# Kernel tuning notes

Hardware: AMD Instinct MI355X
Metric: run time of the kernel (lower is better)

Reference implementation:

```python
import jax, jax.numpy as jnp
from jax import lax
import numpy as np

DIM = 384; NH = 8; N = 16; K = 4; DIN = 768; DTR = 24  # d_model, heads, d_state, d_conv, d_inner, dt_rank
B = 8; Hh = 48; Ww = 48


def _ln(x, g, b):
    m = jnp.mean(x, -1, keepdims=True)
    v = jnp.mean((x - m) ** 2, -1, keepdims=True)
    return (x - m) / jnp.sqrt(v + 1e-5) * g + b


def _mamba(x, in_w, in_b, conv_w, conv_b, xp_w, dt_w, dt_b, A_log, Dp, out_w, out_b):
    # x: (B, L, DIM)
    Bb, L, _ = x.shape
    xz = x @ in_w.T + in_b                      # (B, L, 2*DIN)
    xm, z = xz[..., :DIN], xz[..., DIN:]
    # depthwise causal conv over sequence
    xc = jnp.pad(xm.transpose(0, 2, 1), ((0, 0), (0, 0), (K - 1, 0)))  # (B, DIN, L+K-1)
    xconv = lax.conv_general_dilated(xc, conv_w[:, None, :], (1,), 'VALID',
                                     feature_group_count=DIN,
                                     dimension_numbers=('NCH', 'OIH', 'NCH'))
    u = jax.nn.silu((xconv + conv_b[None, :, None]).transpose(0, 2, 1))  # (B, L, DIN)
    dbc = u @ xp_w.T                            # (B, L, DTR + 2N)
    delta = jax.nn.softplus(dbc[..., :DTR] @ dt_w.T + dt_b)  # (B, L, DIN)
    Bm = dbc[..., DTR:DTR + N]                  # (B, L, N)
    Cm = dbc[..., DTR + N:]                     # (B, L, N)
    A = -jnp.exp(A_log)                         # (DIN, N)

    def step(h, inp):
        d_t, B_t, C_t, u_t = inp                # (B,DIN),(B,N),(B,N),(B,DIN)
        dA = jnp.exp(d_t[:, :, None] * A)       # (B, DIN, N)
        h = h * dA + d_t[:, :, None] * B_t[:, None, :] * u_t[:, :, None]
        y = jnp.einsum('bdn,bn->bd', h, C_t)
        return h, y

    h0 = jnp.zeros((Bb, DIN, N), x.dtype)
    xs = (delta.transpose(1, 0, 2), Bm.transpose(1, 0, 2), Cm.transpose(1, 0, 2), u.transpose(1, 0, 2))
    _, ys = lax.scan(step, h0, xs)
    y = ys.transpose(1, 0, 2) + u * Dp
    y = y * jax.nn.silu(z)
    return y @ out_w.T + out_b


def _forward(x, n1_g, n1_b, ap_w, ap_b, n2_g, n2_b, in_w, in_b, conv_w, conv_b, xp_w, dt_w, dt_b,
             A_log, Dp, out_w, out_b, mod_w1, mod_b1, mod_w2, mod_b2, n3_g, n3_b,
             fc1_w, fc1_b, fc2_w, fc2_b):
    Bb, C, Hc, Wc = x.shape
    xs = x.reshape(Bb, C, Hc * Wc).transpose(0, 2, 1)          # (B, L, C)
    xn = _ln(xs, n1_g, n1_b)
    attn = jax.nn.softmax(xn @ ap_w.T + ap_b, axis=1)          # softmax over sequence
    gc = jnp.einsum('bln,blc->bnc', attn, xn).mean(1)          # (B, C)
    mod = jax.nn.silu(gc @ mod_w1.T + mod_b1) @ mod_w2.T + mod_b2
    xn2 = _ln(xs, n2_g, n2_b)
    mo = _mamba(xn2, in_w, in_b, conv_w, conv_b, xp_w, dt_w, dt_b, A_log, Dp, out_w, out_b)
    mo = mo * (1.0 + mod[:, None, :])
    xs = xs + mo
    h = _ln(xs, n3_g, n3_b)
    h = jax.nn.gelu(h @ fc1_w.T + fc1_b) @ fc2_w.T + fc2_b
    xs = xs + h
    return xs.transpose(0, 2, 1).reshape(Bb, C, Hc, Wc)


def setup_inputs() -> dict:
    key = jax.random.key(0)
    ks = jax.random.split(key, 16)
    s = 0.02
    p = {}
    p['x'] = jax.random.normal(ks[0], (B, DIM, Hh, Ww), jnp.float32)
    p['n1_g'] = jnp.ones((DIM,), jnp.float32); p['n1_b'] = jnp.zeros((DIM,), jnp.float32)
    p['ap_w'] = jax.random.normal(ks[1], (NH, DIM), jnp.float32) * s; p['ap_b'] = jnp.zeros((NH,), jnp.float32)
    p['n2_g'] = jnp.ones((DIM,), jnp.float32); p['n2_b'] = jnp.zeros((DIM,), jnp.float32)
    p['in_w'] = jax.random.normal(ks[2], (2 * DIN, DIM), jnp.float32) * s; p['in_b'] = jnp.zeros((2 * DIN,), jnp.float32)
    p['conv_w'] = jax.random.normal(ks[3], (DIN, K), jnp.float32) * s; p['conv_b'] = jnp.zeros((DIN,), jnp.float32)
    p['xp_w'] = jax.random.normal(ks[4], (DTR + 2 * N, DIN), jnp.float32) * s
    p['dt_w'] = jax.random.normal(ks[5], (DIN, DTR), jnp.float32) * s
    p['dt_b'] = jax.random.uniform(ks[6], (DIN,), jnp.float32, minval=-4.0, maxval=-2.0)
    p['A_log'] = jnp.log(jnp.tile(jnp.arange(1, N + 1, dtype=jnp.float32), (DIN, 1)))
    p['Dp'] = jnp.ones((DIN,), jnp.float32)
    p['out_w'] = jax.random.normal(ks[7], (DIM, DIN), jnp.float32) * s; p['out_b'] = jnp.zeros((DIM,), jnp.float32)
    p['mod_w1'] = jax.random.normal(ks[8], (2 * DIM, DIM), jnp.float32) * s; p['mod_b1'] = jnp.zeros((2 * DIM,), jnp.float32)
    p['mod_w2'] = jax.random.normal(ks[9], (DIM, 2 * DIM), jnp.float32) * s; p['mod_b2'] = jnp.zeros((DIM,), jnp.float32)
    p['n3_g'] = jnp.ones((DIM,), jnp.float32); p['n3_b'] = jnp.zeros((DIM,), jnp.float32)
    p['fc1_w'] = jax.random.normal(ks[10], (4 * DIM, DIM), jnp.float32) * s; p['fc1_b'] = jnp.zeros((4 * DIM,), jnp.float32)
    p['fc2_w'] = jax.random.normal(ks[11], (DIM, 4 * DIM), jnp.float32) * s; p['fc2_b'] = jnp.zeros((DIM,), jnp.float32)
    return p


def reference(x, n1_g, n1_b, ap_w, ap_b, n2_g, n2_b, in_w, in_b, conv_w, conv_b, xp_w, dt_w, dt_b,
              A_log, Dp, out_w, out_b, mod_w1, mod_b1, mod_w2, mod_b2, n3_g, n3_b,
              fc1_w, fc1_b, fc2_w, fc2_b):
    return _forward(x, n1_g, n1_b, ap_w, ap_b, n2_g, n2_b, in_w, in_b, conv_w, conv_b, xp_w,
                    dt_w, dt_b, A_log, Dp, out_w, out_b, mod_w1, mod_b1, mod_w2, mod_b2,
                    n3_g, n3_b, fc1_w, fc1_b, fc2_w, fc2_b)
```

## Files before the change

kernel.cpp:

```cpp
#include <hip/hip_runtime.h>
#include <math.h>

#define DIMC 384
#define NHD 8
#define NSTATE 16
#define DINN 768
#define DTRK 24
#define BB 8
#define LSEQ 2304
#define MROWS (BB*LSEQ)
#define NCH 64
#define TCH 36
#define L2E 1.44269504f

typedef unsigned short u16;
typedef short bf16x8 __attribute__((ext_vector_type(8)));
typedef float f32x4 __attribute__((ext_vector_type(4)));

__device__ __forceinline__ float sigmoid_(float x){ return 1.f/(1.f+__expf(-x)); }
__device__ __forceinline__ float silu_(float x){ return x*sigmoid_(x); }
__device__ __forceinline__ float softplus_(float x){ return (x>20.f)?x:log1pf(__expf(x)); }
__device__ __forceinline__ float gelu_(float x){
  float x3=x*x*x;
  return 0.5f*x*(1.f+tanhf(0.7978845608028654f*(x+0.044715f*x3)));
}
__device__ __forceinline__ float bfu2f(u16 u){
  union{unsigned int i; float f;} c; c.i=((unsigned int)u)<<16; return c.f;
}
__device__ __forceinline__ u16 f2bfu(float f){
  union{float f; unsigned int i;} c; c.f=f;
  unsigned int r = c.i + 0x7FFFu + ((c.i>>16)&1u);
  return (u16)(r>>16);
}
__device__ __forceinline__ void gl_lds16(const u16* g, u16* l){
  __builtin_amdgcn_global_load_lds((__attribute__((address_space(1))) void*)g,
      (__attribute__((address_space(3))) void*)l, 16, 0, 0);
}

#define O1 589824
#define O2 688128
#define O3 983040
#define O4 1572864
#define O5 2162688
#define O6 2187264
#define OEND 2190336
__global__ void k_cvtall(const float* __restrict__ inw, const float* __restrict__ xpw,
    const float* __restrict__ outw, const float* __restrict__ fc1w,
    const float* __restrict__ fc2w, const float* __restrict__ dtw,
    u16* __restrict__ inw_b, u16* __restrict__ xpw_pad, u16* __restrict__ outw_b,
    u16* __restrict__ fc1w_b, u16* __restrict__ fc2w_b, u16* __restrict__ dtw_pad,
    float* __restrict__ gc){
  int i = blockIdx.x*256+threadIdx.x;
  if(i >= OEND) return;
  if(i < O1){ inw_b[i]=f2bfu(inw[i]); }
  else if(i < O2){ int j=i-O1; xpw_pad[j] = (j<43008)? f2bfu(xpw[j]) : (u16)0; }
  else if(i < O3){ int j=i-O2; outw_b[j]=f2bfu(outw[j]); }
  else if(i < O4){ int j=i-O3; fc1w_b[j]=f2bfu(fc1w[j]); }
  else if(i < O5){ int j=i-O4; fc2w_b[j]=f2bfu(fc2w[j]); }
  else if(i < O6){ int j=i-O5; int r=j>>5, c=j&31;
                   dtw_pad[j] = (c<DTRK)? f2bfu(dtw[r*DTRK+c]) : (u16)0; }
  else { gc[i-O6]=0.f; }
}

__global__ void k_transpose(const float* __restrict__ x, float* __restrict__ xs){
  __shared__ float tile[32][33];
  int b = blockIdx.z;
  int t0 = blockIdx.x*32, c0 = blockIdx.y*32;
  int tx = threadIdx.x, ty = threadIdx.y;
  const float* xb = x + (size_t)b*DIMC*LSEQ;
  #pragma unroll
  for(int q=0;q<4;q++)
    tile[ty+q*8][tx] = xb[(size_t)(c0+ty+q*8)*LSEQ + t0+tx];
  __syncthreads();
  float* xsb = xs + (size_t)b*LSEQ*DIMC;
  #pragma unroll
  for(int q=0;q<4;q++)
    xsb[(size_t)(t0+ty+q*8)*DIMC + c0+tx] = tile[tx][ty+q*8];
}

__global__ __launch_bounds__(64) void k_lnstats(const float* __restrict__ xs,
   const float* __restrict__ g1,const float* __restrict__ b1,
   const float* __restrict__ g2,const float* __restrict__ b2,
   const float* __restrict__ apw,const float* __restrict__ apb,
   float* __restrict__ meanr, float* __restrict__ rstdr,
   u16* __restrict__ xn2, float* __restrict__ scores){
  int row = blockIdx.x;
  int lane = threadIdx.x;
  const float* xr = xs + (size_t)row*DIMC;
  float v[6];
  float s=0.f, s2=0.f;
  #pragma unroll
  for(int i=0;i<6;i++){ v[i]=xr[lane+i*64]; s+=v[i]; s2+=v[i]*v[i]; }
  #pragma unroll
  for(int m=32;m>=1;m>>=1){ s += __shfl_xor(s,m); s2 += __shfl_xor(s2,m); }
  float mean = s*(1.f/DIMC);
  float var  = s2*(1.f/DIMC)-mean*mean;
  float rstd = rsqrtf(var+1e-5f);
  if(lane==0){ meanr[row]=mean; rstdr[row]=rstd; }
  float xv1[6];
  #pragma unroll
  for(int i=0;i<6;i++){
    int c = lane+i*64;
    float nx = (v[i]-mean)*rstd;
    xv1[i] = nx*g1[c]+b1[c];
    xn2[(size_t)row*DIMC+c] = f2bfu(nx*g2[c]+b2[c]);
  }
  #pragma unroll
  for(int h=0;h<NHD;h++){
    float p=0.f;
    #pragma unroll
    for(int i=0;i<6;i++) p += xv1[i]*apw[h*DIMC+lane+i*64];
    #pragma unroll
    for(int m=32;m>=1;m>>=1) p += __shfl_xor(p,m);
    if(lane==0) scores[(size_t)row*NHD+h]=p+apb[h];
  }
}

__global__ __launch_bounds__(256) void k_softmax_L(float* __restrict__ sc){
  int bh = blockIdx.x; int b = bh>>3, h = bh&7;
  int tid = threadIdx.x;
  __shared__ float red[8];
  const size_t base = (size_t)b*LSEQ*NHD + h;
  float mx = -1e30f;
  for(int l=tid;l<LSEQ;l+=256) mx = fmaxf(mx, sc[base + (size_t)l*NHD]);
  #pragma unroll
  for(int m=32;m>=1;m>>=1) mx = fmaxf(mx, __shfl_xor(mx,m));
  if((tid&63)==0) red[tid>>6]=mx;
  __syncthreads();
  mx = fmaxf(fmaxf(red[0],red[1]),fmaxf(red[2],red[3]));
  float sum=0.f;
  for(int l=tid;l<LSEQ;l+=256) sum += __expf(sc[base+(size_t)l*NHD]-mx);
  #pragma unroll
  for(int m=32;m>=1;m>>=1) sum += __shfl_xor(sum,m);
  if((tid&63)==0) red[4+(tid>>6)]=sum;
  __syncthreads();
  float inv = 1.f/(red[4]+red[5]+red[6]+red[7]);
  for(int l=tid;l<LSEQ;l+=256){
    size_t idx = base+(size_t)l*NHD;
    sc[idx] = __expf(sc[idx]-mx)*inv;
  }
}

__global__ void k_wpool(const float* __restrict__ attn, float* __restrict__ w){
  int i = blockIdx.x*256+threadIdx.x;
  if(i<MROWS){
    const float* a = attn+(size_t)i*NHD;
    float s=0.f;
    #pragma unroll
    for(int h=0;h<NHD;h++) s+=a[h];
    w[i]=s*0.125f;
  }
}

__global__ __launch_bounds__(384) void k_gc(const float* __restrict__ w,
    const float* __restrict__ xs, const float* __restrict__ meanr,
    const float* __restrict__ rstdr, const float* __restrict__ g1,
    const float* __restrict__ b1, float* __restrict__ gc){
  int b = blockIdx.x; int chunk = blockIdx.y; int c = threadIdx.x;
  int l0 = chunk*48;
  float acc=0.f, accw=0.f;
  for(int l=0;l<48;l++){
    int row = b*LSEQ + l0+l;
    float ww = w[row];
    acc  += ww*(xs[(size_t)row*DIMC+c]-meanr[row])*rstdr[row];
    accw += ww;
  }
  atomicAdd(&gc[b*DIMC+c], acc*g1[c]+accw*b1[c]);
}

__global__ __launch_bounds__(64) void k_mod1(const float* __restrict__ gc,
    const float* __restrict__ w1, const float* __restrict__ b1, float* __restrict__ h){
  int b = blockIdx.x; int n = blockIdx.y*64+threadIdx.x;
  const float* g = gc + b*DIMC;
  const float* wr = w1 + (size_t)n*DIMC;
  float acc=0.f;
  for(int k=0;k<DIMC;k++) acc += g[k]*wr[k];
  h[b*768+n] = silu_(acc+b1[n]);
}
__global__ __launch_bounds__(64) void k_mod2(const float* __restrict__ h,
    const float* __restrict__ w2, const float* __restrict__ b2, float* __restrict__ mod){
  int b = blockIdx.x; int n = blockIdx.y*64+threadIdx.x;
  const float* hh = h + b*768;
  const float* wr = w2 + (size_t)n*768;
  float acc=0.f;
  for(int k=0;k<768;k++) acc += hh[k]*wr[k];
  mod[b*DIMC+n] = acc+b2[n];
}

template<int EPI>
__global__ __launch_bounds__(256,4) void k_mgemm(
    const u16* __restrict__ A, const u16* __restrict__ W,
    const float* __restrict__ bias, void* __restrict__ outp,
    int K, int N, const float* __restrict__ aux, void* __restrict__ outp2)
{
  __shared__ u16 lA[2][4096];
  __shared__ u16 lB[2][4096];
  int tid = threadIdx.x;
  int m0 = blockIdx.x*128, n0 = blockIdx.y*128;
  int wid = tid>>6, lane = tid&63;
  int wr = wid>>1, wc = wid&1;
  int lrow = lane&15, lk = lane>>4;
  f32x4 acc[4][4];
  #pragma unroll
  for(int i=0;i<4;i++)
    #pragma unroll
    for(int j=0;j<4;j++){ acc[i][j][0]=0.f; acc[i][j][1]=0.f; acc[i][j][2]=0.f; acc[i][j][3]=0.f; }

  int r0 = tid & 127, k0 = tid >> 7;
  const u16* Ag0 = A + (size_t)(m0+r0)*K + k0*8;
  const u16* Ag1 = A + (size_t)(m0+r0)*K + (k0+2)*8;
  const u16* Bg0 = W + (size_t)(n0+r0)*K + k0*8;
  const u16* Bg1 = W + (size_t)(n0+r0)*K + (k0+2)*8;

  gl_lds16(Ag0, &lA[0][tid*8]);
  gl_lds16(Ag1, &lA[0][2048+tid*8]);
  gl_lds16(Bg0, &lB[0][tid*8]);
  gl_lds16(Bg1, &lB[0][2048+tid*8]);
  if(32 < K){
    gl_lds16(Ag0+32, &lA[1][tid*8]);
    gl_lds16(Ag1+32, &lA[1][2048+tid*8]);
    gl_lds16(Bg0+32, &lB[1][tid*8]);
    gl_lds16(Bg1+32, &lB[1][2048+tid*8]);
  }

  int cur = 0;
  for(int kb=0; kb<K; kb+=32){
    if(kb+32 < K) asm volatile("s_waitcnt vmcnt(4)" ::: "memory");
    else          asm volatile("s_waitcnt vmcnt(0)" ::: "memory");
    __builtin_amdgcn_s_barrier();
    bf16x8 af[4], bfr[4];
    #pragma unroll
    for(int i=0;i<4;i++){
      af[i]  = *reinterpret_cast<const bf16x8*>(&lA[cur][(lk*128 + wr*64 + i*16 + lrow)*8]);
      bfr[i] = *reinterpret_cast<const bf16x8*>(&lB[cur][(lk*128 + wc*64 + i*16 + lrow)*8]);
    }
    asm volatile("s_waitcnt lgkmcnt(0)" ::: "memory");
    __builtin_amdgcn_s_barrier();
    if(kb+64 < K){
      gl_lds16(Ag0 + kb+64, &lA[cur][tid*8]);
      gl_lds16(Ag1 + kb+64, &lA[cur][2048+tid*8]);
      gl_lds16(Bg0 + kb+64, &lB[cur][tid*8]);
      gl_lds16(Bg1 + kb+64, &lB[cur][2048+tid*8]);
    }
    #pragma unroll
    for(int i=0;i<4;i++)
      #pragma unroll
      for(int j=0;j<4;j++)
        acc[i][j] = __builtin_amdgcn_mfma_f32_16x16x32_bf16(af[i], bfr[j], acc[i][j], 0,0,0);
    cur ^= 1;
  }

  #pragma unroll
  for(int i=0;i<4;i++){
    int row = m0 + wr*64 + i*16 + lk*4;
    #pragma unroll
    for(int j=0;j<4;j++){
      int col = n0 + wc*64 + j*16 + lrow;
      float bc = bias ? bias[col] : 0.f;
      f32x4 v = acc[i][j];
      if(EPI==0){
        u16* o = (u16*)outp;
        #pragma unroll
        for(int r=0;r<4;r++) o[(size_t)(row+r)*N + col] = f2bfu(v[r]+bc);
      } else if(EPI==1){
        u16* o = (u16*)outp;
        #pragma unroll
        for(int r=0;r<4;r++) o[(size_t)(row+r)*N + col] = f2bfu(gelu_(v[r]+bc));
      } else if(EPI==2){
        float* o = (float*)outp;
        int bi = row/LSEQ;
        float sc = 1.f + aux[bi*DIMC + col];
        #pragma unroll
        for(int r=0;r<4;r++) o[(size_t)(row+r)*DIMC + col] += (v[r]+bc)*sc;
      } else if(EPI==3){
        float* o = (float*)outp;
        int bi = row/LSEQ, t = row - bi*LSEQ;
        float4 s;
        s.x = aux[(size_t)(row+0)*DIMC+col] + v[0] + bc;
        s.y = aux[(size_t)(row+1)*DIMC+col] + v[1] + bc;
        s.z = aux[(size_t)(row+2)*DIMC+col] + v[2] + bc;
        s.w = aux[(size_t)(row+3)*DIMC+col] + v[3] + bc;
        *reinterpret_cast<float4*>(&o[((size_t)(bi*DIMC+col))*LSEQ + t]) = s;
      } else if(EPI==4){
        float* o = (float*)outp;
        if(col < N){
          #pragma unroll
          for(int r=0;r<4;r++) o[(size_t)(row+r)*N + col] = v[r]+bc;
        }
      } else if(EPI==5){
        u16* o = (col < 768) ? (u16*)outp : (u16*)outp2;
        int cc = (col < 768) ? col : col - 768;
        #pragma unroll
        for(int r=0;r<4;r++) o[(size_t)(row+r)*768 + cc] = f2bfu(v[r]+bc);
      } else if(EPI==6){
        float* o = (float*)outp;
        u16* o2 = (u16*)outp2;
        #pragma unroll
        for(int r=0;r<4;r++){
          float val = v[r];
          if(col < 56) o[(size_t)(row+r)*56 + col] = val;
          if(col < 32) o2[(size_t)(row+r)*32 + col] = (col<DTRK)? f2bfu(val) : (u16)0;
        }
      } else {
        u16* o = (u16*)outp;
        #pragma unroll
        for(int r=0;r<4;r++) o[(size_t)(row+r)*N + col] = f2bfu(softplus_(v[r]+bc));
      }
    }
  }
}

__global__ void k_conv(const u16* __restrict__ xm, const float* __restrict__ cw,
                       const float* __restrict__ cb, u16* __restrict__ u){
  int idx = blockIdx.x*256+threadIdx.x;
  if(idx >= MROWS*(DINN/8)) return;
  int j = idx % (DINN/8); int r = idx / (DINN/8);
  int t = r % LSEQ; int d0 = j*8;
  float4 w4_[8];
  #pragma unroll
  for(int e=0;e<8;e++) w4_[e] = reinterpret_cast<const float4*>(cw)[d0+e];
  float acc[8];
  #pragma unroll
  for(int e=0;e<8;e++) acc[e]=cb[d0+e];
  #pragma unroll
  for(int k=0;k<4;k++){
    int tt=t+k-3;
    if(tt>=0){
      uint4 v = *reinterpret_cast<const uint4*>(&xm[(size_t)(r+k-3)*DINN + d0]);
      unsigned vv[4]={v.x,v.y,v.z,v.w};
      #pragma unroll
      for(int e=0;e<8;e++){
        u16 raw = (e&1)? (u16)(vv[e>>1]>>16) : (u16)(vv[e>>1]&0xffffu);
        float wk = (k==0)? w4_[e].x : (k==1)? w4_[e].y : (k==2)? w4_[e].z : w4_[e].w;
        acc[e] += bfu2f(raw)*wk;
      }
    }
  }
  u16 outv[8];
  #pragma unroll
  for(int e=0;e<8;e++) outv[e]=f2bfu(silu_(acc[e]));
  *reinterpret_cast<uint4*>(&u[(size_t)r*DINN+d0]) = *reinterpret_cast<const uint4*>(outv);
}

__global__ __launch_bounds__(256) void k_scan1(
  const u16* __restrict__ dt_, const u16* __restrict__ u_,
  const float* __restrict__ dbc, const float* __restrict__ alog,
  float* __restrict__ ssum, float* __restrict__ hloc)
{
  __shared__ float Bsh[TCH][16];
  int bid = blockIdx.x;
  int b = bid/(NCH*3); int rem = bid%(NCH*3); int ch = rem/3; int dblk = rem%3;
  int tid = threadIdx.x; int d = dblk*256 + tid;
  size_t rbase = (size_t)b*LSEQ + (size_t)ch*TCH;
  for(int j=tid; j<TCH*16; j+=256){
    int row=j>>4, n=j&15;
    Bsh[row][n] = dbc[(rbase+row)*56 + DTRK + n];
  }
  float Acl2[16];
  float a0 = -__expf(alog[(size_t)d*16])*L2E;
  bool fast = true;
  #pragma unroll
  for(int n=0;n<16;n++){
    Acl2[n] = -__expf(alog[(size_t)d*16+n])*L2E;
    float tgt = (float)(n+1)*a0;
    fast = fast && (fabsf(Acl2[n]-tgt) <= 1e-4f*fabsf(tgt));
  }
  float h[16];
  #pragma unroll
  for(int n=0;n<16;n++) h[n]=0.f;
  float S=0.f;
  const u16* dtp = dt_ + rbase*DINN + d;
  const u16* up  = u_  + rbase*DINN + d;
  __syncthreads();
  if(fast){
    for(int t=0;t<TCH;t++){
      float dt = bfu2f(dtp[(size_t)t*DINN]);
      float uv = bfu2f(up[(size_t)t*DINN]);
      float G = dt*uv;
      S += dt;
      float e = exp2f(dt*a0), w = e;
      const float4* b4 = (const float4*)Bsh[t];
      float4 B0=b4[0],B1=b4[1],B2=b4[2],B3=b4[3];
      float Bv[16]={B0.x,B0.y,B0.z,B0.w,B1.x,B1.y,B1.z,B1.w,
                    B2.x,B2.y,B2.z,B2.w,B3.x,B3.y,B3.z,B3.w};
      #pragma unroll
      for(int n=0;n<16;n++){ h[n] = h[n]*w + G*Bv[n]; w *= e; }
    }
  } else {
    for(int t=0;t<TCH;t++){
      float dt = bfu2f(dtp[(size_t)t*DINN]);
      float uv = bfu2f(up[(size_t)t*DINN]);
      float G = dt*uv;
      S += dt;
      const float4* b4 = (const float4*)Bsh[t];
      float4 B0=b4[0],B1=b4[1],B2=b4[2],B3=b4[3];
      float Bv[16]={B0.x,B0.y,B0.z,B0.w,B1.x,B1.y,B1.z,B1.w,
                    B2.x,B2.y,B2.z,B2.w,B3.x,B3.y,B3.z,B3.w};
      #pragma unroll
      for(int n=0;n<16;n++) h[n] = h[n]*exp2f(dt*Acl2[n]) + G*Bv[n];
    }
  }
  ssum[((size_t)b*NCH+ch)*DINN + d] = S;
  float* hp = hloc + (((size_t)b*NCH+ch)*DINN + d)*16;
  #pragma unroll
  for(int n=0;n<16;n++) hp[n] = h[n];
}

__global__ __launch_bounds__(256) void k_scan2(
  const float* __restrict__ ssum, const float* __restrict__ alog,
  float* __restrict__ hl)
{
  int gid = blockIdx.x*256+threadIdx.x;
  int n = gid & 15; int d = (gid>>4)%DINN; int b = gid/(DINN*NSTATE);
  float Acl2 = -__expf(alog[(size_t)d*16+n])*L2E;
  float hin=0.f;
  for(int ch=0; ch<NCH; ch++){
    size_t sidx = ((size_t)b*NCH+ch)*DINN + d;
    size_t idx  = sidx*16 + n;
    float a = exp2f(ssum[sidx]*Acl2);
    float hold = hl[idx];
    hl[idx] = hin;
    hin = a*hin + hold;
  }
}

__global__ __launch_bounds__(256) void k_scan3(
  const u16* __restrict__ dt_, u16* uy, const u16* __restrict__ z_,
  const float* __restrict__ dbc, const float* __restrict__ alog,
  const float* __restrict__ Dp, const float* __restrict__ hin)
{
  __shared__ float BC[TCH][32];
  int bid = blockIdx.x;
  int b = bid/(NCH*3); int rem = bid%(NCH*3); int ch = rem/3; int dblk = rem%3;
  int tid = threadIdx.x; int d = dblk*256 + tid;
  size_t rbase = (size_t)b*LSEQ + (size_t)ch*TCH;
  for(int j=tid; j<TCH*32; j+=256){
    int row=j>>5, c=j&31;
    BC[row][c] = dbc[(rbase+row)*56 + DTRK + c];
  }
  float Acl2[16], h[16];
  const float* hp = hin + (((size_t)b*NCH+ch)*DINN + d)*16;
  float a0 = -__expf(alog[(size_t)d*16])*L2E;
  bool fast = true;
  #pragma unroll
  for(int n=0;n<16;n++){
    Acl2[n] = -__expf(alog[(size_t)d*16+n])*L2E;
    float tgt = (float)(n+1)*a0;
    fast = fast && (fabsf(Acl2[n]-tgt) <= 1e-4f*fabsf(tgt));
    h[n] = hp[n];
  }
  float Dv = Dp[d];
  const u16* dtp = dt_ + rbase*DINN + d;
  u16*       uyp = uy  + rbase*DINN + d;
  const u16* zp  = z_  + rbase*DINN + d;
  __syncthreads();
  if(fast){
    for(int t=0;t<TCH;t++){
      float dt = bfu2f(dtp[(size_t)t*DINN]);
      float uv = bfu2f(uyp[(size_t)t*DINN]);
      float zv = bfu2f(zp[(size_t)t*DINN]);
      float G = dt*uv;
      float e = exp2f(dt*a0), w = e;
      const float4* bc4 = (const float4*)BC[t];
      float4 B0=bc4[0],B1=bc4[1],B2=bc4[2],B3=bc4[3];
      float4 C0=bc4[4],C1=bc4[5],C2=bc4[6],C3=bc4[7];
      float Bv[16]={B0.x,B0.y,B0.z,B0.w,B1.x,B1.y,B1.z,B1.w,
                    B2.x,B2.y,B2.z,B2.w,B3.x,B3.y,B3.z,B3.w};
      float Cv[16]={C0.x,C0.y,C0.z,C0.w,C1.x,C1.y,C1.z,C1.w,
                    C2.x,C2.y,C2.z,C2.w,C3.x,C3.y,C3.z,C3.w};
      float y0=0.f,y1=0.f,y2=0.f,y3=0.f;
      #pragma unroll
      for(int n=0;n<16;n++){
        h[n] = h[n]*w + G*Bv[n];
        w *= e;
        if((n&3)==0) y0 += h[n]*Cv[n];
        else if((n&3)==1) y1 += h[n]*Cv[n];
        else if((n&3)==2) y2 += h[n]*Cv[n];
        else y3 += h[n]*Cv[n];
      }
      float y = (y0+y1)+(y2+y3);
      uyp[(size_t)t*DINN] = f2bfu((y + uv*Dv)*silu_(zv));
    }
  } else {
    for(int t=0;t<TCH;t++){
      float dt = bfu2f(dtp[(size_t)t*DINN]);
      float uv = bfu2f(uyp[(size_t)t*DINN]);
      float zv = bfu2f(zp[(size_t)t*DINN]);
      float G = dt*uv;
      const float4* bc4 = (const float4*)BC[t];
      float4 B0=bc4[0],B1=bc4[1],B2=bc4[2],B3=bc4[3];
      float4 C0=bc4[4],C1=bc4[5],C2=bc4[6],C3=bc4[7];
      float Bv[16]={B0.x,B0.y,B0.z,B0.w,B1.x,B1.y,B1.z,B1.w,
                    B2.x,B2.y,B2.z,B2.w,B3.x,B3.y,B3.z,B3.w};
      float Cv[16]={C0.x,C0.y,C0.z,C0.w,C1.x,C1.y,C1.z,C1.w,
                    C2.x,C2.y,C2.z,C2.w,C3.x,C3.y,C3.z,C3.w};
      float y0=0.f,y1=0.f,y2=0.f,y3=0.f;
      #pragma unroll
      for(int n=0;n<16;n++){
        h[n] = h[n]*exp2f(dt*Acl2[n]) + G*Bv[n];
        if((n&3)==0) y0 += h[n]*Cv[n];
        else if((n&3)==1) y1 += h[n]*Cv[n];
        else if((n&3)==2) y2 += h[n]*Cv[n];
        else y3 += h[n]*Cv[n];
      }
      float y = (y0+y1)+(y2+y3);
      uyp[(size_t)t*DINN] = f2bfu((y + uv*Dv)*silu_(zv));
    }
  }
}

__global__ __launch_bounds__(64) void k_ln3(const float* __restrict__ xin,
    const float* __restrict__ g, const float* __restrict__ bb, u16* __restrict__ xout){
  int row = blockIdx.x;
  int lane = threadIdx.x;
  const float* xr = xin + (size_t)row*DIMC;
  float v[6];
  float s=0.f, s2=0.f;
  #pragma unroll
  for(int i=0;i<6;i++){ v[i]=xr[lane+i*64]; s+=v[i]; s2+=v[i]*v[i]; }
  #pragma unroll
  for(int m=32;m>=1;m>>=1){ s += __shfl_xor(s,m); s2 += __shfl_xor(s2,m); }
  float mean = s*(1.f/DIMC);
  float var  = s2*(1.f/DIMC)-mean*mean;
  float rstd = rsqrtf(var+1e-5f);
  #pragma unroll
  for(int i=0;i<6;i++){
    int c = lane+i*64;
    xout[(size_t)row*DIMC+c] = f2bfu((v[i]-mean)*rstd*g[c]+bb[c]);
  }
}

extern "C" void kernel_launch(void* const* d_in, const int* in_sizes, int n_in,
                              void* d_out, int out_size, void* d_ws, size_t ws_size,
                              hipStream_t stream)
{
  const float* x     = (const float*)d_in[0];
  const float* n1g   = (const float*)d_in[1];
  const float* n1b   = (const float*)d_in[2];
  const float* apw   = (const float*)d_in[3];
  const float* apb   = (const float*)d_in[4];
  const float* n2g   = (const float*)d_in[5];
  const float* n2b   = (const float*)d_in[6];
  const float* inw   = (const float*)d_in[7];
  const float* inb   = (const float*)d_in[8];
  const float* convw = (const float*)d_in[9];
  const float* convb = (const float*)d_in[10];
  const float* xpw   = (const float*)d_in[11];
  const float* dtw   = (const float*)d_in[12];
  const float* dtb   = (const float*)d_in[13];
  const float* Alog  = (const float*)d_in[14];
  const float* Dp    = (const float*)d_in[15];
  const float* outw  = (const float*)d_in[16];
  const float* outb  = (const float*)d_in[17];
  const float* modw1 = (const float*)d_in[18];
  const float* modb1 = (const float*)d_in[19];
  const float* modw2 = (const float*)d_in[20];
  const float* modb2 = (const float*)d_in[21];
  const float* n3g   = (const float*)d_in[22];
  const float* n3b   = (const float*)d_in[23];
  const float* fc1w  = (const float*)d_in[24];
  const float* fc1b  = (const float*)d_in[25];
  const float* fc2w  = (const float*)d_in[26];
  const float* fc2b  = (const float*)d_in[27];

  float* ws = (float*)d_ws;
  float* XS    = ws;
  float* R1    = ws + 7077888;
  u16*   XMb   = (u16*)R1;
  u16*   DTb   = (u16*)R1;
  float* SSUM  = R1 + 7077888;
  float* HL    = R1 + 7471104;
  u16*   F1b   = (u16*)R1;
  u16*   Zb    = (u16*)(ws + 21233664);
  float* DBC   = ws + 28311552;
  float* WB    = ws + 29343744;
  u16*   inw_b   = (u16*)WB;
  u16*   xpw_pad = inw_b + 589824;
  u16*   outw_b  = xpw_pad + 98304;
  u16*   fc1w_b  = outw_b + 294912;
  u16*   fc2w_b  = fc1w_b + 589824;
  float* SCORES= ws + 30425088;
  float* WPOOL = ws + 30572544;
  float* MEANR = ws + 30590976;
  float* RSTDR = ws + 30609408;
  float* GC    = ws + 30627840;
  float* MODH  = ws + 30630912;
  float* MOD   = ws + 30637056;
  u16*   DT32b = (u16*)(ws + 30640128);
  u16*   dtw_pad=(u16*)(ws + 30935040);
  (void)ws_size; (void)n_in; (void)in_sizes; (void)out_size;

  u16* XN2b = (u16*)d_out;
  u16* Ub   = (u16*)d_out;
  u16* Hb   = (u16*)d_out;

  k_cvtall<<<(OEND+255)/256, 256, 0, stream>>>(inw, xpw, outw, fc1w, fc2w, dtw,
      inw_b, xpw_pad, outw_b, fc1w_b, fc2w_b, dtw_pad, GC);

  k_transpose<<<dim3(72,12,8), dim3(32,8), 0, stream>>>(x, XS);
  k_lnstats<<<MROWS, 64, 0, stream>>>(XS, n1g,n1b,n2g,n2b, apw,apb, MEANR, RSTDR, XN2b, SCORES);
  k_softmax_L<<<BB*NHD, 256, 0, stream>>>(SCORES);
  k_wpool<<<(MROWS+255)/256, 256, 0, stream>>>(SCORES, WPOOL);
  k_gc<<<dim3(BB,48), 384, 0, stream>>>(WPOOL, XS, MEANR, RSTDR, n1g, n1b, GC);
  k_mod1<<<dim3(BB,12), 64, 0, stream>>>(GC, modw1, modb1, MODH);
  k_mod2<<<dim3(BB,6), 64, 0, stream>>>(MODH, modw2, modb2, MOD);

  k_mgemm<5><<<dim3(144,12), 256, 0, stream>>>(XN2b, inw_b, inb, XMb, 384, 1536, nullptr, Zb);
  k_conv<<<(MROWS*(DINN/8)+255)/256, 256, 0, stream>>>(XMb, convw, convb, Ub);
  k_mgemm<6><<<dim3(144,1), 256, 0, stream>>>(Ub, xpw_pad, nullptr, DBC, 768, 56, nullptr, DT32b);
  k_mgemm<7><<<dim3(144,6), 256, 0, stream>>>(DT32b, dtw_pad, dtb, DTb, 32, 768, nullptr, nullptr);
  k_scan1<<<BB*NCH*3, 256, 0, stream>>>(DTb, Ub, DBC, Alog, SSUM, HL);
  k_scan2<<<384, 256, 0, stream>>>(SSUM, Alog, HL);
  k_scan3<<<BB*NCH*3, 256, 0, stream>>>(DTb, Ub, Zb, DBC, Alog, Dp, HL);
  k_mgemm<2><<<dim3(144,3), 256, 0, stream>>>(Ub, outw_b, outb, XS, 768, 384, MOD, nullptr);
  k_ln3<<<MROWS, 64, 0, stream>>>(XS, n3g, n3b, Hb);
  k_mgemm<1><<<dim3(144,12), 256, 0, stream>>>(Hb, fc1w_b, fc1b, F1b, 384, 1536, nullptr, nullptr);
  k_mgemm<3><<<dim3(144,3), 256, 0, stream>>>(F1b, fc2w_b, fc2b, d_out, 1536, 384, XS, nullptr);
}
```

Before: 533.9 us.

## Pre-swizzle GEMM weights into MFMA fragment layout and load B directly from global

Weights are converted to bf16 in a tiled layout that matches the MFMA B-fragment order, so each GEMM wave loads its B fragments straight from global memory and the LDS staging for B goes away. This halves LDS use and removes the barrier-synchronised B copies, but B now comes from global/L2 with no shared reuse, which adds latency on the critical path. Two smaller changes ride along: the head-pooling kernel is folded into k_gc, and the two modulation MLP kernels become one per-batch kernel that keeps the hidden vector in shared memory. The single-block-per-batch modulation kernel runs with much less parallelism than before.

```diff
diff --git a/kernel.cpp b/kernel.cpp
--- a/kernel.cpp
+++ b/kernel.cpp
@@ -35,6 +35,15 @@
 __device__ __forceinline__ void gl_lds16(const u16* g, u16* l){
   __builtin_amdgcn_global_load_lds((__attribute__((address_space(1))) void*)g,
       (__attribute__((address_space(3))) void*)l, 16, 0, 0);
+}
+
+__device__ __forceinline__ u16 swzw(const float* __restrict__ s, int o, int KT,
+                                    int Nsrc, int Ksrc){
+  int e = o&7, l = (o>>3)&63, rest = o>>9;
+  int kt = rest % KT, nt = rest / KT;
+  int n = nt*16 + (l&15);
+  int k = kt*32 + ((l>>4)<<3) + e;
+  return (n<Nsrc && k<Ksrc) ? f2bfu(s[(size_t)n*Ksrc + k]) : (u16)0;
 }
 
 #define O1 589824
@@ -52,13 +61,12 @@
     float* __restrict__ gc){
   int i = blockIdx.x*256+threadIdx.x;
   if(i >= OEND) return;
-  if(i < O1){ inw_b[i]=f2bfu(inw[i]); }
-  else if(i < O2){ int j=i-O1; xpw_pad[j] = (j<43008)? f2bfu(xpw[j]) : (u16)0; }
-  else if(i < O3){ int j=i-O2; outw_b[j]=f2bfu(outw[j]); }
-  else if(i < O4){ int j=i-O3; fc1w_b[j]=f2bfu(fc1w[j]); }
-  else if(i < O5){ int j=i-O4; fc2w_b[j]=f2bfu(fc2w[j]); }
-  else if(i < O6){ int j=i-O5; int r=j>>5, c=j&31;
-                   dtw_pad[j] = (c<DTRK)? f2bfu(dtw[r*DTRK+c]) : (u16)0; }
+  if(i < O1){ inw_b[i]   = swzw(inw,  i,    12, 1536, 384); }
+  else if(i < O2){ xpw_pad[i-O1] = swzw(xpw,  i-O1, 24, 56,   768); }
+  else if(i < O3){ outw_b[i-O2]  = swzw(outw, i-O2, 24, 384,  768); }
+  else if(i < O4){ fc1w_b[i-O3]  = swzw(fc1w, i-O3, 12, 1536, 384); }
+  else if(i < O5){ fc2w_b[i-O4]  = swzw(fc2w, i-O4, 48, 384,  1536); }
+  else if(i < O6){ dtw_pad[i-O5] = swzw(dtw,  i-O5, 1,  768,  24); }
   else { gc[i-O6]=0.f; }
 }
 
@@ -141,18 +149,7 @@
   }
 }
 
-__global__ void k_wpool(const float* __restrict__ attn, float* __restrict__ w){
-  int i = blockIdx.x*256+threadIdx.x;
-  if(i<MROWS){
-    const float* a = attn+(size_t)i*NHD;
-    float s=0.f;
-    #pragma unroll
-    for(int h=0;h<NHD;h++) s+=a[h];
-    w[i]=s*0.125f;
-  }
-}
-
-__global__ __launch_bounds__(384) void k_gc(const float* __restrict__ w,
+__global__ __launch_bounds__(384) void k_gc(const float* __restrict__ attn,
     const float* __restrict__ xs, const float* __restrict__ meanr,
     const float* __restrict__ rstdr, const float* __restrict__ g1,
     const float* __restrict__ b1, float* __restrict__ gc){
@@ -161,40 +158,43 @@
   float acc=0.f, accw=0.f;
   for(int l=0;l<48;l++){
     int row = b*LSEQ + l0+l;
-    float ww = w[row];
+    const float* a = attn + (size_t)row*NHD;
+    float ww = (((a[0]+a[1])+(a[2]+a[3]))+((a[4]+a[5])+(a[6]+a[7])))*0.125f;
     acc  += ww*(xs[(size_t)row*DIMC+c]-meanr[row])*rstdr[row];
     accw += ww;
   }
   atomicAdd(&gc[b*DIMC+c], acc*g1[c]+accw*b1[c]);
 }
 
-__global__ __launch_bounds__(64) void k_mod1(const float* __restrict__ gc,
-    const float* __restrict__ w1, const float* __restrict__ b1, float* __restrict__ h){
-  int b = blockIdx.x; int n = blockIdx.y*64+threadIdx.x;
+__global__ __launch_bounds__(256) void k_mod(const float* __restrict__ gc,
+    const float* __restrict__ w1, const float* __restrict__ b1,
+    const float* __restrict__ w2, const float* __restrict__ b2,
+    float* __restrict__ mod){
+  __shared__ float hsh[768];
+  int b = blockIdx.x, tid = threadIdx.x;
   const float* g = gc + b*DIMC;
-  const float* wr = w1 + (size_t)n*DIMC;
-  float acc=0.f;
-  for(int k=0;k<DIMC;k++) acc += g[k]*wr[k];
-  h[b*768+n] = silu_(acc+b1[n]);
-}
-__global__ __launch_bounds__(64) void k_mod2(const float* __restrict__ h,
-    const float* __restrict__ w2, const float* __restrict__ b2, float* __restrict__ mod){
-  int b = blockIdx.x; int n = blockIdx.y*64+threadIdx.x;
-  const float* hh = h + b*768;
-  const float* wr = w2 + (size_t)n*768;
-  float acc=0.f;
-  for(int k=0;k<768;k++) acc += hh[k]*wr[k];
-  mod[b*DIMC+n] = acc+b2[n];
+  for(int n=tid; n<768; n+=256){
+    const float* wr = w1 + (size_t)n*DIMC;
+    float acc=0.f;
+    for(int k=0;k<DIMC;k++) acc += g[k]*wr[k];
+    hsh[n] = silu_(acc+b1[n]);
+  }
+  __syncthreads();
+  for(int n=tid; n<DIMC; n+=256){
+    const float* wr = w2 + (size_t)n*768;
+    float acc=0.f;
+    for(int k=0;k<768;k++) acc += hsh[k]*wr[k];
+    mod[b*DIMC+n] = acc+b2[n];
+  }
 }
 
 template<int EPI>
 __global__ __launch_bounds__(256,4) void k_mgemm(
-    const u16* __restrict__ A, const u16* __restrict__ W,
+    const u16* __restrict__ A, const u16* __restrict__ Wf,
     const float* __restrict__ bias, void* __restrict__ outp,
     int K, int N, const float* __restrict__ aux, void* __restrict__ outp2)
 {
   __shared__ u16 lA[2][4096];
-  __shared__ u16 lB[2][4096];
   int tid = threadIdx.x;
   int m0 = blockIdx.x*128, n0 = blockIdx.y*128;
   int wid = tid>>6, lane = tid&63;
@@ -209,38 +209,35 @@
   int r0 = tid & 127, k0 = tid >> 7;
   const u16* Ag0 = A + (size_t)(m0+r0)*K + k0*8;
   const u16* Ag1 = A + (size_t)(m0+r0)*K + (k0+2)*8;
-  const u16* Bg0 = W + (size_t)(n0+r0)*K + k0*8;
-  const u16* Bg1 = W + (size_t)(n0+r0)*K + (k0+2)*8;
+  const int KT = K >> 5;
+  const u16* Wfb = Wf + ((size_t)((n0>>4) + wc*4)*KT)*512 + (size_t)lane*8;
 
   gl_lds16(Ag0, &lA[0][tid*8]);
   gl_lds16(Ag1, &lA[0][2048+tid*8]);
-  gl_lds16(Bg0, &lB[0][tid*8]);
-  gl_lds16(Bg1, &lB[0][2048+tid*8]);
   if(32 < K){
     gl_lds16(Ag0+32, &lA[1][tid*8]);
     gl_lds16(Ag1+32, &lA[1][2048+tid*8]);
-    gl_lds16(Bg0+32, &lB[1][tid*8]);
-    gl_lds16(Bg1+32, &lB[1][2048+tid*8]);
   }
 
   int cur = 0;
   for(int kb=0; kb<K; kb+=32){
-    if(kb+32 < K) asm volatile("s_waitcnt vmcnt(4)" ::: "memory");
+    int kt = kb>>5;
+    if(kb+32 < K) asm volatile("s_waitcnt vmcnt(2)" ::: "memory");
     else          asm volatile("s_waitcnt vmcnt(0)" ::: "memory");
     __builtin_amdgcn_s_barrier();
-    bf16x8 af[4], bfr[4];
+    bf16x8 bfr[4];
     #pragma unroll
-    for(int i=0;i<4;i++){
-      af[i]  = *reinterpret_cast<const bf16x8*>(&lA[cur][(lk*128 + wr*64 + i*16 + lrow)*8]);
-      bfr[i] = *reinterpret_cast<const bf16x8*>(&lB[cur][(lk*128 + wc*64 + i*16 + lrow)*8]);
-    }
+    for(int j=0;j<4;j++)
+      bfr[j] = *reinterpret_cast<const bf16x8*>(Wfb + ((size_t)j*KT + kt)*512);
+    bf16x8 af[4];
+    #pragma unroll
+    for(int i=0;i<4;i++)
+      af[i] = *reinterpret_cast<const bf16x8*>(&lA[cur][(lk*128 + wr*64 + i*16 + lrow)*8]);
     asm volatile("s_waitcnt lgkmcnt(0)" ::: "memory");
     __builtin_amdgcn_s_barrier();
     if(kb+64 < K){
       gl_lds16(Ag0 + kb+64, &lA[cur][tid*8]);
       gl_lds16(Ag1 + kb+64, &lA[cur][2048+tid*8]);
-      gl_lds16(Bg0 + kb+64, &lB[cur][tid*8]);
-      gl_lds16(Bg1 + kb+64, &lB[cur][2048+tid*8]);
     }
     #pragma unroll
     for(int i=0;i<4;i++)
@@ -580,11 +577,9 @@
   u16*   fc1w_b  = outw_b + 294912;
   u16*   fc2w_b  = fc1w_b + 589824;
   float* SCORES= ws + 30425088;
-  float* WPOOL = ws + 30572544;
   float* MEANR = ws + 30590976;
   float* RSTDR = ws + 30609408;
   float* GC    = ws + 30627840;
-  float* MODH  = ws + 30630912;
   float* MOD   = ws + 30637056;
   u16*   DT32b = (u16*)(ws + 30640128);
   u16*   dtw_pad=(u16*)(ws + 30935040);
@@ -600,10 +595,8 @@
   k_transpose<<<dim3(72,12,8), dim3(32,8), 0, stream>>>(x, XS);
   k_lnstats<<<MROWS, 64, 0, stream>>>(XS, n1g,n1b,n2g,n2b, apw,apb, MEANR, RSTDR, XN2b, SCORES);
   k_softmax_L<<<BB*NHD, 256, 0, stream>>>(SCORES);
-  k_wpool<<<(MROWS+255)/256, 256, 0, stream>>>(SCORES, WPOOL);
-  k_gc<<<dim3(BB,48), 384, 0, stream>>>(WPOOL, XS, MEANR, RSTDR, n1g, n1b, GC);
-  k_mod1<<<dim3(BB,12), 64, 0, stream>>>(GC, modw1, modb1, MODH);
-  k_mod2<<<dim3(BB,6), 64, 0, stream>>>(MODH, modw2, modb2, MOD);
+  k_gc<<<dim3(BB,48), 384, 0, stream>>>(SCORES, XS, MEANR, RSTDR, n1g, n1b, GC);
+  k_mod<<<BB, 256, 0, stream>>>(GC, modw1, modb1, modw2, modb2, MOD);
 
   k_mgemm<5><<<dim3(144,12), 256, 0, stream>>>(XN2b, inw_b, inb, XMb, 384, 1536, nullptr, Zb);
   k_conv<<<(MROWS*(DINN/8)+255)/256, 256, 0, stream>>>(XMb, convw, convb, Ub);
```

New measurement: 555.4 us. +4.0%, slower.
